# Optimization experiments

Measured on AMD Instinct MI355X. Metric: run time of the kernel, lower is better.

## Reference

```python
import jax, jax.numpy as jnp
import numpy as np
from jax import lax

HEADS = 8
EPS = 1e-5


def _ln2d(x, g, b):
    # LayerNorm over channel axis of BCHW (torch LayerNorm(dim) after b c h w -> b h w c)
    mu = jnp.mean(x, axis=1, keepdims=True)
    var = jnp.mean(jnp.square(x - mu), axis=1, keepdims=True)
    xn = (x - mu) * lax.rsqrt(var + EPS)
    return xn * g[None, :, None, None] + b[None, :, None, None]


def _conv1x1(x, w, b):
    # w: [out_c, in_c]
    return jnp.einsum('bchw,oc->bohw', x, w) + b[None, :, None, None]


def _dwconv3x3(x, w, b):
    # w: [C, 1, 3, 3], depthwise
    y = lax.conv_general_dilated(x, w, window_strides=(1, 1), padding='SAME',
                                 feature_group_count=x.shape[1],
                                 dimension_numbers=('NCHW', 'OIHW', 'NCHW'))
    return y + b[None, :, None, None]


def _gelu(x):
    return jax.nn.gelu(x, approximate=False)


def _linear_attention(x, qkv_w, qkv_b, out_w, out_b):
    B, C, H, W = x.shape
    hd = C // HEADS
    qkv = _conv1x1(x, qkv_w, qkv_b)              # [B, 3C, H, W]
    q, k, v = jnp.split(qkv, 3, axis=1)
    # b (h c) h0 w0 -> b h c (h0 w0)
    q = q.reshape(B, HEADS, hd, H * W)
    k = k.reshape(B, HEADS, hd, H * W)
    v = v.reshape(B, HEADS, hd, H * W)
    q = jax.nn.softmax(q, axis=2)                # over head_dim
    k = jax.nn.softmax(k, axis=3)                # over pixels
    context = jnp.einsum('bhcn,bhdn->bhcd', k, v)  # [B, H, hd, hd]
    out = jnp.einsum('bhcd,bhcn->bhdn', context, q)  # [B, H, hd, N]
    out = out.reshape(B, C, H, W)
    return _conv1x1(out, out_w, out_b)


def _ffn(x, w1, b1, dw_w, dw_b, w2, b2):
    h = _gelu(_conv1x1(x, w1, b1))
    h = _gelu(_dwconv3x3(h, dw_w, dw_b))
    return _conv1x1(h, w2, b2)


def setup_inputs() -> dict:
    key = jax.random.key(0)
    ks = jax.random.split(key, 6)
    B, C, H, W = 4, 192, 256, 256
    hidden = C * 2
    s = 0.02
    return {
        'x': jax.random.normal(ks[0], (B, C, H, W), jnp.float32),
        'ln1_g': jnp.ones((C,), jnp.float32),
        'ln1_b': jnp.zeros((C,), jnp.float32),
        'qkv_w': jax.random.normal(ks[1], (3 * C, C), jnp.float32) * s,
        'qkv_b': jnp.zeros((3 * C,), jnp.float32),
        'out_w': jax.random.normal(ks[2], (C, C), jnp.float32) * s,
        'out_b': jnp.zeros((C,), jnp.float32),
        'ln2_g': jnp.ones((C,), jnp.float32),
        'ln2_b': jnp.zeros((C,), jnp.float32),
        'w1': jax.random.normal(ks[3], (hidden, C), jnp.float32) * s,
        'b1': jnp.zeros((hidden,), jnp.float32),
        'dw_w': jax.random.normal(ks[4], (hidden, 1, 3, 3), jnp.float32) * s,
        'dw_b': jnp.zeros((hidden,), jnp.float32),
        'w2': jax.random.normal(ks[5], (C, hidden), jnp.float32) * s,
        'b2': jnp.zeros((C,), jnp.float32),
    }


def reference(x, ln1_g, ln1_b, qkv_w, qkv_b, out_w, out_b, ln2_g, ln2_b, w1, b1, dw_w, dw_b, w2, b2):
    x = x + _linear_attention(_ln2d(x, ln1_g, ln1_b), qkv_w, qkv_b, out_w, out_b)
    x = x + _ffn(_ln2d(x, ln2_g, ln2_b), w1, b1, dw_w, dw_b, w2, b2)
    return x
```

## Files before the change

kernel.cpp:

```cpp
#include <hip/hip_runtime.h>
#include <math.h>

typedef __attribute__((ext_vector_type(8))) short s8;
typedef __attribute__((ext_vector_type(8))) unsigned short us8;
typedef __attribute__((ext_vector_type(4))) float f4;
typedef __attribute__((ext_vector_type(4))) unsigned short us4;
typedef __attribute__((ext_vector_type(4))) unsigned int u32x4;

#define DEVI __device__ __forceinline__

static const int NPIX = 65536;

DEVI float b2f(unsigned short u) {
    unsigned int v = ((unsigned int)u) << 16;
    float f; __builtin_memcpy(&f, &v, 4); return f;
}
DEVI unsigned short f2b(float f) {
    unsigned int u; __builtin_memcpy(&u, &f, 4);
    unsigned int r = (u + 0x7FFFu + ((u >> 16) & 1u)) >> 16;
    return (unsigned short)r;
}
DEVI float geluf(float x) { return 0.5f * x * (1.0f + erff(x * 0.70710678118f)); }
DEVI float gelu_t(float x) {
    float z = 1.595769122f * (x + 0.044715f * x * x * x);
    return x * __builtin_amdgcn_rcpf(1.0f + __expf(-z));
}
DEVI float rfl(float v) {
    int i; __builtin_memcpy(&i, &v, 4);
    i = __builtin_amdgcn_readfirstlane(i);
    float o; __builtin_memcpy(&o, &i, 4); return o;
}

DEVI void gload_lds16(const unsigned short* g, unsigned short* l) {
    __builtin_amdgcn_global_load_lds(
        (const __attribute__((address_space(1))) unsigned int*)g,
        (__attribute__((address_space(3))) unsigned int*)l,
        16, 0, 0);
}

__global__ __launch_bounds__(256) void lnt_k(const float* __restrict__ X,
                                             const float* __restrict__ gw,
                                             const float* __restrict__ gb,
                                             unsigned short* __restrict__ Out)
{
    const int i = blockIdx.x * 256 + threadIdx.x;
    const int b = i >> 16, px = i & 65535;
    const float* xp = X + (size_t)b * 192 * NPIX + px;

    unsigned int pk[96];
    float sum = 0.f, ssq = 0.f;
    #pragma unroll
    for (int c = 0; c < 192; c++) {
        float v = xp[(size_t)c * NPIX];
        sum += v; ssq += v * v;
        unsigned int h = f2b(v);
        if (c & 1) pk[c >> 1] |= h << 16;
        else       pk[c >> 1] = h;
    }
    float mu = sum * (1.0f / 192.0f);
    float var = ssq * (1.0f / 192.0f) - mu * mu;
    float rs = rsqrtf(var + 1e-5f);

    #pragma unroll
    for (int c2 = 0; c2 < 96; c2++) {
        int c = c2 * 2;
        float lo = b2f((unsigned short)(pk[c2] & 0xFFFF));
        float hi = b2f((unsigned short)(pk[c2] >> 16));
        lo = (lo - mu) * rs * gw[c] + gb[c];
        hi = (hi - mu) * rs * gw[c + 1] + gb[c + 1];
        pk[c2] = (unsigned int)f2b(lo) | ((unsigned int)f2b(hi) << 16);
    }
    u32x4* dst = (u32x4*)(Out + (size_t)i * 192);
    #pragma unroll
    for (int j = 0; j < 6; j++) {
        u32x4 v = { pk[4 * j], pk[4 * j + 1], pk[4 * j + 2], pk[4 * j + 3] };
        dst[j] = v;
    }
}

template<int MODE, int NCHUNK, int UNITS, int NTILE>
__global__ __launch_bounds__(256) void gemm3_k(
    const unsigned short* __restrict__ X, const unsigned short* __restrict__ Wb,
    const float* __restrict__ bias, const void* __restrict__ resid,
    void* __restrict__ Out, int OCTOT, unsigned short* __restrict__ qT)
{
    constexpr int KTOT = UNITS * 192;
    __shared__ unsigned short tile[2][64 * 192];

    const int tid = threadIdx.x;
    const int wave = tid >> 6, lane = tid & 63;
    const int lr = lane & 15, lg = lane >> 4;
    const int xr = lr & 7;

    auto stage = [&](int s, int buf) {
        const int t = s / UNITS, u = s - t * UNITS;
        const int gp0s = (blockIdx.x * NTILE + t) * 64;
        const unsigned short* Xb = X + (size_t)gp0s * KTOT + u * 192;
        #pragma unroll
        for (int j = 0; j < 6; j++) {
            int ci = (wave * 6 + j) * 64 + lane;
            int row = ci / 24;
            int c = ci - row * 24;
            int csw = (c & ~7) | ((c ^ row) & 7);
            gload_lds16(Xb + (size_t)row * KTOT + csw * 8, &tile[buf][ci * 8]);
        }
    };

    stage(0, 0);

    for (int t = 0; t < NTILE; t++) {
        const int gp0 = (blockIdx.x * NTILE + t) * 64;
        const int b = gp0 >> 16;
        const int pxb = gp0 & 65535;

        if constexpr (UNITS == 1) {
            __syncthreads();
            if (t + 1 < NTILE) stage(t + 1, (t + 1) & 1);
            const unsigned short* tb = tile[t & 1];

            #pragma unroll
            for (int cn = 0; cn < NCHUNK; cn++) {
                const int ocb = cn * 192 + wave * 48;
                const unsigned short* wrow = Wb + (size_t)(ocb + lr) * KTOT + lg * 8;
                const bool swapped = (MODE == 1) || (MODE == 3 && cn == 0);

                s8 wf[3][6];
                #pragma unroll
                for (int ot = 0; ot < 3; ot++)
                    #pragma unroll
                    for (int kk = 0; kk < 6; kk++)
                        wf[ot][kk] = *(const s8*)(wrow + (size_t)ot * 16 * KTOT + kk * 32);

                f4 acc[4][3];
                #pragma unroll
                for (int i = 0; i < 4; i++)
                    #pragma unroll
                    for (int j = 0; j < 3; j++) acc[i][j] = (f4)0.0f;

                #pragma unroll
                for (int kk = 0; kk < 6; kk++) {
                    const int kc = kk * 4 + lg;
                    const int kcs = (kc & ~7) | ((kc ^ xr) & 7);
                    s8 a[4];
                    #pragma unroll
                    for (int pt = 0; pt < 4; pt++)
                        a[pt] = *(const s8*)&tb[((pt * 16 + lr) * 24 + kcs) * 8];
                    #pragma unroll
                    for (int ot = 0; ot < 3; ot++)
                        #pragma unroll
                        for (int pt = 0; pt < 4; pt++)
                            acc[pt][ot] = swapped
                                ? __builtin_amdgcn_mfma_f32_16x16x32_bf16(wf[ot][kk], a[pt], acc[pt][ot], 0, 0, 0)
                                : __builtin_amdgcn_mfma_f32_16x16x32_bf16(a[pt], wf[ot][kk], acc[pt][ot], 0, 0, 0);
                }

                if (MODE == 3 && cn == 0) {
                    #pragma unroll
                    for (int pt = 0; pt < 4; pt++) {
                        const int gp = gp0 + pt * 16 + lr;
                        unsigned short* orow = qT + (size_t)gp * 192 + wave * 48 + lg * 4;
                        #pragma unroll
                        for (int ot = 0; ot < 3; ot++) {
                            f4 bi4 = *(const f4*)&bias[wave * 48 + ot * 16 + lg * 4];
                            us4 o;
                            #pragma unroll
                            for (int r = 0; r < 4; r++) o[r] = f2b(acc[pt][ot][r] + bi4[r]);
                            *(us4*)(orow + ot * 16) = o;
                        }
                    }
                } else if (MODE == 3) {
                    #pragma unroll
                    for (int ot = 0; ot < 3; ot++) {
                        const int oc = ocb + ot * 16 + lr;
                        const float bi = bias[oc];
                        const size_t rowoff = ((size_t)b * 384 + (oc - 192)) * NPIX + pxb + lg * 4;
                        #pragma unroll
                        for (int pt = 0; pt < 4; pt++) {
                            us4 o;
                            #pragma unroll
                            for (int r = 0; r < 4; r++) o[r] = f2b(acc[pt][ot][r] + bi);
                            *(us4*)((unsigned short*)Out + rowoff + pt * 16) = o;
                        }
                    }
                } else {
                    #pragma unroll
                    for (int pt = 0; pt < 4; pt++) {
                        const int gp = gp0 + pt * 16 + lr;
                        unsigned short* orow = (unsigned short*)Out + (size_t)gp * OCTOT + ocb + lg * 4;
                        #pragma unroll
                        for (int ot = 0; ot < 3; ot++) {
                            f4 bi4 = *(const f4*)&bias[ocb + ot * 16 + lg * 4];
                            us4 o;
                            #pragma unroll
                            for (int r = 0; r < 4; r++) o[r] = f2b(geluf(acc[pt][ot][r] + bi4[r]));
                            *(us4*)(orow + ot * 16) = o;
                        }
                    }
                }
            }
        } else {
            const int ocb = wave * 48;
            const unsigned short* wrow = Wb + (size_t)(ocb + lr) * KTOT + lg * 8;

            f4 acc[4][3];
            #pragma unroll
            for (int i = 0; i < 4; i++)
                #pragma unroll
                for (int j = 0; j < 3; j++) acc[i][j] = (f4)0.0f;

            #pragma unroll
            for (int u = 0; u < 2; u++) {
                const int s = t * 2 + u;
                __syncthreads();
                if (s + 1 < NTILE * 2) stage(s + 1, (s + 1) & 1);
                const unsigned short* tb = tile[s & 1];

                s8 wf[3][6];
                #pragma unroll
                for (int ot = 0; ot < 3; ot++)
                    #pragma unroll
                    for (int kk = 0; kk < 6; kk++)
                        wf[ot][kk] = *(const s8*)(wrow + (size_t)ot * 16 * KTOT + u * 192 + kk * 32);

                #pragma unroll
                for (int kk = 0; kk < 6; kk++) {
                    const int kc = kk * 4 + lg;
                    const int kcs = (kc & ~7) | ((kc ^ xr) & 7);
                    s8 a[4];
                    #pragma unroll
                    for (int pt = 0; pt < 4; pt++)
                        a[pt] = *(const s8*)&tb[((pt * 16 + lr) * 24 + kcs) * 8];
                    #pragma unroll
                    for (int ot = 0; ot < 3; ot++)
                        #pragma unroll
                        for (int pt = 0; pt < 4; pt++)
                            acc[pt][ot] = __builtin_amdgcn_mfma_f32_16x16x32_bf16(a[pt], wf[ot][kk], acc[pt][ot], 0, 0, 0);
                }
            }

            #pragma unroll
            for (int ot = 0; ot < 3; ot++) {
                const int oc = ocb + ot * 16 + lr;
                const float bi = bias[oc];
                const size_t rowoff = ((size_t)b * 192 + oc) * NPIX + pxb + lg * 4;
                #pragma unroll
                for (int pt = 0; pt < 4; pt++) {
                    if (MODE == 2) {
                        f4 rv = *(const f4*)((const float*)resid + rowoff + pt * 16);
                        f4 o;
                        #pragma unroll
                        for (int r = 0; r < 4; r++) o[r] = acc[pt][ot][r] + bi + rv[r];
                        *(f4*)((float*)Out + rowoff + pt * 16) = o;
                    } else {
                        us4 rv = *(const us4*)((const unsigned short*)resid + rowoff + pt * 16);
                        f4 o;
                        #pragma unroll
                        for (int r = 0; r < 4; r++) o[r] = acc[pt][ot][r] + bi + b2f(rv[r]);
                        *(f4*)((float*)Out + rowoff + pt * 16) = o;
                    }
                }
            }
        }
    }
}

__global__ __launch_bounds__(256) void krow_k(const unsigned short* __restrict__ kv,
                                              float* __restrict__ koff)
{
    int r = blockIdx.x;
    int b = r / 192, ch = r % 192;
    const unsigned short* Kp = kv + ((size_t)b * 384 + ch) * NPIX;
    int tid = threadIdx.x;
    float m0 = -1e30f, s0 = 0.f, m1 = -1e30f, s1 = 0.f;
    for (int i = 0; i < 128; i++) {
        float v0 = b2f(Kp[tid + (size_t)(2 * i) * 256]);
        float v1 = b2f(Kp[tid + (size_t)(2 * i + 1) * 256]);
        if (v0 > m0) { s0 = s0 * __expf(m0 - v0) + 1.f; m0 = v0; }
        else s0 += __expf(v0 - m0);
        if (v1 > m1) { s1 = s1 * __expf(m1 - v1) + 1.f; m1 = v1; }
        else s1 += __expf(v1 - m1);
    }
    float m = fmaxf(m0, m1);
    float s = s0 * __expf(m0 - m) + s1 * __expf(m1 - m);
    __shared__ float ms[256], ss[256];
    ms[tid] = m; ss[tid] = s;
    __syncthreads();
    for (int off = 128; off > 0; off >>= 1) {
        if (tid < off) {
            float m2 = ms[tid + off], s2 = ss[tid + off];
            float M2 = fmaxf(ms[tid], m2);
            ss[tid] = ss[tid] * __expf(ms[tid] - M2) + s2 * __expf(m2 - M2);
            ms[tid] = M2;
        }
        __syncthreads();
    }
    if (tid == 0) koff[r] = ms[0] + logf(ss[0]);
}

__global__ void zero_k(float* __restrict__ p, int n)
{
    int i = blockIdx.x * 256 + threadIdx.x;
    if (i < n) p[i] = 0.f;
}

__global__ void cvt_k(const float* __restrict__ src, unsigned short* __restrict__ dst, int n)
{
    int i = blockIdx.x * 256 + threadIdx.x;
    if (i < n) dst[i] = f2b(src[i]);
}

__global__ __launch_bounds__(256) void context_k(const unsigned short* __restrict__ kv,
                                                 const float* __restrict__ koff,
                                                 float* __restrict__ ctxT)
{
    __shared__ float red[4][64][16];
    int bid = blockIdx.x;
    int bh = bid >> 4, cgrp = bid & 15;
    int b = bh >> 3, h = bh & 7;
    int tid = threadIdx.x;
    int wave = tid >> 6, lane = tid & 63, lr = lane & 15, lg = lane >> 4;
    int chunk = cgrp * 4 + wave;
    size_t nbase = (size_t)chunk * 1024 + lg * 8;

    int c0 = h * 24 + lr;
    int c1 = h * 24 + 16 + lr;
    float ko0 = koff[b * 192 + c0];
    int i1 = b * 192 + c1; if (i1 > 767) i1 = 767;
    float ko1 = koff[i1];
    bool val1 = lr < 8;

    const unsigned short* k0p = kv + ((size_t)b * 384 + c0) * NPIX + nbase;
    const unsigned short* k1p = kv + ((size_t)b * 384 + (c1 > 191 ? 191 : c1)) * NPIX + nbase;
    const unsigned short* v0p = kv + ((size_t)b * 384 + 192 + h * 24 + lr) * NPIX + nbase;
    const unsigned short* v1p = kv + ((size_t)b * 384 + 192 + ((h * 24 + 16 + lr > 191) ? 191 : h * 24 + 16 + lr)) * NPIX + nbase;

    f4 acc[2][2];
    #pragma unroll
    for (int i = 0; i < 2; i++) for (int j = 0; j < 2; j++) acc[i][j] = (f4)0.0f;

    for (int s = 0; s < 32; s++) {
        int off = s * 32;
        s8 kr0 = *(const s8*)(k0p + off);
        s8 kr1 = *(const s8*)(k1p + off);
        s8 vr0 = *(const s8*)(v0p + off);
        s8 vr1 = *(const s8*)(v1p + off);
        s8 p0, p1;
        #pragma unroll
        for (int j = 0; j < 8; j++) {
            p0[j] = (short)f2b(__expf(b2f((unsigned short)kr0[j]) - ko0));
            p1[j] = val1 ? (short)f2b(__expf(b2f((unsigned short)kr1[j]) - ko1)) : (short)0;
        }
        acc[0][0] = __builtin_amdgcn_mfma_f32_16x16x32_bf16(p0, vr0, acc[0][0], 0, 0, 0);
        acc[0][1] = __builtin_amdgcn_mfma_f32_16x16x32_bf16(p0, vr1, acc[0][1], 0, 0, 0);
        acc[1][0] = __builtin_amdgcn_mfma_f32_16x16x32_bf16(p1, vr0, acc[1][0], 0, 0, 0);
        acc[1][1] = __builtin_amdgcn_mfma_f32_16x16x32_bf16(p1, vr1, acc[1][1], 0, 0, 0);
    }
    #pragma unroll
    for (int mt = 0; mt < 2; mt++)
        #pragma unroll
        for (int ct = 0; ct < 2; ct++)
            #pragma unroll
            for (int r = 0; r < 4; r++)
                red[wave][lane][mt * 8 + ct * 4 + r] = acc[mt][ct][r];
    __syncthreads();

    if (wave == 0) {
        float* base = ctxT + (size_t)(b * 8 + h) * 1024;
        #pragma unroll
        for (int j = 0; j < 16; j++) {
            float sum = red[0][lane][j] + red[1][lane][j] + red[2][lane][j] + red[3][lane][j];
            int mt = j >> 3, ct = (j >> 2) & 1, r = j & 3;
            int c = mt * 16 + lg * 4 + r;
            int d = ct * 16 + lr;
            atomicAdd(base + d * 32 + c, sum);
        }
    }
}

template<bool BIGWS>
__global__ __launch_bounds__(256) void qctx_proj_k(
    const unsigned short* __restrict__ qT, const float* __restrict__ ctxT,
    const unsigned short* __restrict__ outWb, const float* __restrict__ outBias,
    const float* __restrict__ xres, float* __restrict__ Out,
    unsigned short* __restrict__ x2b,
    const float* __restrict__ ln2g, const float* __restrict__ ln2b,
    unsigned short* __restrict__ xnt)
{
    __shared__ unsigned short outp[64][200];
    __shared__ float lnS[4][64], lnQ[4][64];

    int tid = threadIdx.x, bid = blockIdx.x;
    int b = bid >> 10, n0 = (bid & 1023) * 64;
    int wave = tid >> 6, lane = tid & 63, lr = lane & 15, lg = lane >> 4;
    const size_t bpx = (size_t)b << 16;

    #pragma unroll
    for (int hh = 0; hh < 2; hh++) {
        int h = wave * 2 + hh;
        s8 cf[2];
        #pragma unroll
        for (int mt = 0; mt < 2; mt++) {
            const float* cp = ctxT + ((size_t)(b * 8 + h) * 32 + mt * 16 + lr) * 32 + lg * 8;
            s8 a;
            #pragma unroll
            for (int j = 0; j < 8; j++) a[j] = (short)f2b(cp[j]);
            cf[mt] = a;
        }
        #pragma unroll
        for (int nt = 0; nt < 4; nt++) {
            int n = nt * 16 + lr;
            s8 bfq = (s8)0;
            float sown = 0.f;
            if (lg < 3) {
                us8 qv = *(const us8*)(qT + (bpx + n0 + n) * 192 + h * 24 + lg * 8);
                #pragma unroll
                for (int j = 0; j < 8; j++) {
                    float e = __expf(b2f((unsigned short)qv[j]));
                    sown += e;
                    bfq[j] = (short)f2b(e);
                }
            }
            float den = sown;
            den += __shfl_xor(den, 16);
            den += __shfl_xor(den, 32);
            f4 z = (f4)0.0f;
            f4 d0 = __builtin_amdgcn_mfma_f32_16x16x32_bf16(cf[0], bfq, z, 0, 0, 0);
            f4 d1 = __builtin_amdgcn_mfma_f32_16x16x32_bf16(cf[1], bfq, z, 0, 0, 0);
            float sinv = 1.0f / den;
            us4 w0;
            #pragma unroll
            for (int r = 0; r < 4; r++) w0[r] = f2b(d0[r] * sinv);
            *(us4*)&outp[n][h * 24 + lg * 4] = w0;
            if (lg < 2) {
                us4 w1;
                #pragma unroll
                for (int r = 0; r < 4; r++) w1[r] = f2b(d1[r] * sinv);
                *(us4*)&outp[n][h * 24 + 16 + lg * 4] = w1;
            }
        }
    }
    __syncthreads();

    f4 acc[4][3];
    #pragma unroll
    for (int i = 0; i < 4; i++) for (int j = 0; j < 3; j++) acc[i][j] = (f4)0.0f;
    #pragma unroll
    for (int k0 = 0; k0 < 192; k0 += 32) {
        s8 bf[4];
        #pragma unroll
        for (int pt = 0; pt < 4; pt++)
            bf[pt] = *(const s8*)&outp[pt * 16 + lr][k0 + lg * 8];
        #pragma unroll
        for (int ot = 0; ot < 3; ot++) {
            s8 af = *(const s8*)&outWb[(size_t)(wave * 48 + ot * 16 + lr) * 192 + k0 + lg * 8];
            #pragma unroll
            for (int pt = 0; pt < 4; pt++)
                acc[pt][ot] = __builtin_amdgcn_mfma_f32_16x16x32_bf16(bf[pt], af, acc[pt][ot], 0, 0, 0);
        }
    }

    float sP[4][4], qP[4][4];
    #pragma unroll
    for (int pt = 0; pt < 4; pt++)
        #pragma unroll
        for (int r = 0; r < 4; r++) { sP[pt][r] = 0.f; qP[pt][r] = 0.f; }

    #pragma unroll
    for (int ot = 0; ot < 3; ot++) {
        const int oc = wave * 48 + ot * 16 + lr;
        const float bi = outBias[oc];
        const size_t rowbase = ((size_t)b * 192 + oc) * NPIX + n0 + lg * 4;
        #pragma unroll
        for (int pt = 0; pt < 4; pt++) {
            f4 rv = *(const f4*)(xres + rowbase + pt * 16);
            f4 v;
            #pragma unroll
            for (int r = 0; r < 4; r++) {
                v[r] = acc[pt][ot][r] + bi + rv[r];
                sP[pt][r] += v[r]; qP[pt][r] += v[r] * v[r];
            }
            acc[pt][ot] = v;
            if (BIGWS) {
                us4 o;
                #pragma unroll
                for (int r = 0; r < 4; r++) o[r] = f2b(v[r]);
                *(us4*)(x2b + rowbase + pt * 16) = o;
            } else {
                *(f4*)(Out + rowbase + pt * 16) = v;
            }
        }
    }
    #pragma unroll
    for (int pt = 0; pt < 4; pt++)
        #pragma unroll
        for (int r = 0; r < 4; r++) {
            float s = sP[pt][r], q = qP[pt][r];
            s += __shfl_xor(s, 1); s += __shfl_xor(s, 2);
            s += __shfl_xor(s, 4); s += __shfl_xor(s, 8);
            q += __shfl_xor(q, 1); q += __shfl_xor(q, 2);
            q += __shfl_xor(q, 4); q += __shfl_xor(q, 8);
            sP[pt][r] = s; qP[pt][r] = q;
        }
    if (lr == 0) {
        #pragma unroll
        for (int pt = 0; pt < 4; pt++)
            #pragma unroll
            for (int r = 0; r < 4; r++) {
                lnS[wave][pt * 16 + lg * 4 + r] = sP[pt][r];
                lnQ[wave][pt * 16 + lg * 4 + r] = qP[pt][r];
            }
    }
    __syncthreads();

    float lgv[3], lbv[3];
    #pragma unroll
    for (int ot = 0; ot < 3; ot++) {
        int oc = wave * 48 + ot * 16 + lr;
        lgv[ot] = ln2g[oc]; lbv[ot] = ln2b[oc];
    }
    #pragma unroll
    for (int pt = 0; pt < 4; pt++) {
        float mu4[4], rs4[4];
        #pragma unroll
        for (int r = 0; r < 4; r++) {
            int px = pt * 16 + lg * 4 + r;
            float S = lnS[0][px] + lnS[1][px] + lnS[2][px] + lnS[3][px];
            float Qq = lnQ[0][px] + lnQ[1][px] + lnQ[2][px] + lnQ[3][px];
            float mu = S * (1.0f / 192.0f);
            float var = Qq * (1.0f / 192.0f) - mu * mu;
            mu4[r] = mu; rs4[r] = rsqrtf(var + 1e-5f);
        }
        #pragma unroll
        for (int ot = 0; ot < 3; ot++) {
            int oc = wave * 48 + ot * 16 + lr;
            #pragma unroll
            for (int r = 0; r < 4; r++) {
                int px = pt * 16 + lg * 4 + r;
                float xn = (acc[pt][ot][r] - mu4[r]) * rs4[r] * lgv[ot] + lbv[ot];
                outp[px][oc] = f2b(xn);
            }
        }
    }
    __syncthreads();

    #pragma unroll
    for (int q = 0; q < 6; q++) {
        int idx = q * 256 + tid;
        int px = idx / 24, c8 = idx % 24;
        us8 v = *(const us8*)&outp[px][c8 * 8];
        *(us8*)(xnt + (bpx + n0 + px) * 192 + c8 * 8) = v;
    }
}

__global__ __launch_bounds__(256) void dwconv_t2_k(
    const unsigned short* __restrict__ h1t, const float* __restrict__ w,
    const float* __restrict__ bias, unsigned short* __restrict__ h2t)
{
    __shared__ unsigned short ring[4 * 4 * 66 * 8];
    const int bz = blockIdx.z;
    const int b = bz / 12, cb = (bz % 12) * 32;
    const int y0 = blockIdx.y * 8, x0 = blockIdx.x * 64;
    const int tid = threadIdx.x;
    const int x = tid & 63, cg = tid >> 6;
    const int c0 = cb + cg * 8;
    const size_t bbase = (size_t)b << 16;

    float wr[9][8], bi[8];
    #pragma unroll
    for (int i = 0; i < 8; i++) {
        #pragma unroll
        for (int j = 0; j < 9; j++) wr[j][i] = rfl(w[(c0 + i) * 9 + j]);
        bi[i] = rfl(bias[c0 + i]);
    }

    const us8 zz = {0, 0, 0, 0, 0, 0, 0, 0};

    auto stage_row = [&](int gy, int s) {
        unsigned short* ldsrow = &ring[((s * 4 + cg) * 66) * 8];
        if (gy >= 0 && gy <= 255) {
            us8 ev = zz;
            if (x == 0 && x0 > 0)
                ev = *(const us8*)(h1t + (bbase + gy * 256 + x0 - 1) * 384 + c0);
            if (x == 63 && x0 + 64 < 256)
                ev = *(const us8*)(h1t + (bbase + gy * 256 + x0 + 64) * 384 + c0);
            gload_lds16(h1t + (bbase + gy * 256 + x0 + x) * 384 + c0,
                        ldsrow + (1 + x) * 8);
            if (x == 0)  *(us8*)&ldsrow[0]      = ev;
            if (x == 63) *(us8*)&ldsrow[65 * 8] = ev;
        } else {
            *(us8*)&ldsrow[(1 + x) * 8] = zz;
            if (x == 0)  *(us8*)&ldsrow[0]      = zz;
            if (x == 63) *(us8*)&ldsrow[65 * 8] = zz;
        }
    };

    stage_row(y0 - 1, 0);
    stage_row(y0,     1);
    stage_row(y0 + 1, 2);
    __syncthreads();

    #pragma unroll
    for (int y = 0; y < 8; y++) {
        if (y < 7) stage_row(y0 + y + 2, (y + 3) & 3);

        float a[8];
        #pragma unroll
        for (int i = 0; i < 8; i++) a[i] = bi[i];
        #pragma unroll
        for (int t = 0; t < 3; t++) {
            const int s = (y + t) & 3;
            const unsigned short* rp = &ring[((s * 4 + cg) * 66 + x) * 8];
            us8 L = *(const us8*)(rp);
            us8 C = *(const us8*)(rp + 8);
            us8 R = *(const us8*)(rp + 16);
            #pragma unroll
            for (int i = 0; i < 8; i++) {
                a[i] += wr[t * 3 + 0][i] * b2f(L[i]);
                a[i] += wr[t * 3 + 1][i] * b2f(C[i]);
                a[i] += wr[t * 3 + 2][i] * b2f(R[i]);
            }
        }
        us8 ov;
        #pragma unroll
        for (int i = 0; i < 8; i++) ov[i] = f2b(gelu_t(a[i]));
        *(us8*)(h2t + (bbase + (y0 + y) * 256 + x0 + x) * 384 + c0) = ov;

        __syncthreads();
    }
}

extern "C" void kernel_launch(void* const* d_in, const int* in_sizes, int n_in,
                              void* d_out, int out_size, void* d_ws, size_t ws_size,
                              hipStream_t stream)
{
    const float* x    = (const float*)d_in[0];
    const float* ln1g = (const float*)d_in[1];
    const float* ln1b = (const float*)d_in[2];
    const float* qkvw = (const float*)d_in[3];
    const float* qkvb = (const float*)d_in[4];
    const float* outw = (const float*)d_in[5];
    const float* outb = (const float*)d_in[6];
    const float* ln2g = (const float*)d_in[7];
    const float* ln2b = (const float*)d_in[8];
    const float* w1   = (const float*)d_in[9];
    const float* b1   = (const float*)d_in[10];
    const float* dww  = (const float*)d_in[11];
    const float* dwb  = (const float*)d_in[12];
    const float* w2   = (const float*)d_in[13];
    const float* b2   = (const float*)d_in[14];
    float* out = (float*)d_out;

    char* ws = (char*)d_ws;
    unsigned short* kv  = (unsigned short*)ws;
    unsigned short* h1t = (unsigned short*)ws;
    unsigned short* h2t = (unsigned short*)(ws + (size_t)201326592);
    unsigned short* qT  = (unsigned short*)(ws + (size_t)201326592);
    unsigned short* xnt = (unsigned short*)(ws + (size_t)301989888);
    size_t off = (size_t)402653184;
    float* koff = (float*)(ws + off); off += 4096;
    float* ctxT = (float*)(ws + off); off += 131072;
    unsigned short* qkvwb = (unsigned short*)(ws + off); off += 221184;
    unsigned short* outwb = (unsigned short*)(ws + off); off += 73728 * 2;
    unsigned short* w1b   = (unsigned short*)(ws + off); off += 147456;
    unsigned short* w2b   = (unsigned short*)(ws + off); off += 147456;
    off = (off + 255) & ~(size_t)255;
    unsigned short* x2b = (unsigned short*)(ws + off);
    const bool bigws = ws_size >= off + (size_t)100663296;

    cvt_k<<<(110592 + 255) / 256, 256, 0, stream>>>(qkvw, qkvwb, 110592);
    cvt_k<<<(36864 + 255) / 256, 256, 0, stream>>>(outw, outwb, 36864);
    cvt_k<<<(73728 + 255) / 256, 256, 0, stream>>>(w1, w1b, 73728);
    cvt_k<<<(73728 + 255) / 256, 256, 0, stream>>>(w2, w2b, 73728);

    lnt_k<<<1024, 256, 0, stream>>>(x, ln1g, ln1b, xnt);

    gemm3_k<3, 3, 1, 4><<<1024, 256, 0, stream>>>(xnt, qkvwb, qkvb, nullptr, kv, 384, qT);

    krow_k<<<768, 256, 0, stream>>>(kv, koff);

    zero_k<<<128, 256, 0, stream>>>(ctxT, 32768);
    context_k<<<512, 256, 0, stream>>>(kv, koff, ctxT);

    if (bigws)
        qctx_proj_k<true><<<4096, 256, 0, stream>>>(qT, ctxT, outwb, outb, x, out,
                                                    x2b, ln2g, ln2b, xnt);
    else
        qctx_proj_k<false><<<4096, 256, 0, stream>>>(qT, ctxT, outwb, outb, x, out,
                                                     x2b, ln2g, ln2b, xnt);

    gemm3_k<1, 2, 1, 4><<<1024, 256, 0, stream>>>(xnt, w1b, b1, nullptr, h1t, 384, nullptr);

    dwconv_t2_k<<<dim3(4, 32, 48), 256, 0, stream>>>(h1t, dww, dwb, h2t);

    if (bigws)
        gemm3_k<4, 1, 2, 4><<<1024, 256, 0, stream>>>(h2t, w2b, b2, x2b, out, 192, nullptr);
    else
        gemm3_k<2, 1, 2, 4><<<1024, 256, 0, stream>>>(h2t, w2b, b2, out, out, 192, nullptr);
}
```

Before: 971.7 us.

## Process two pixel tiles per block in qctx_proj with async Q staging; taller dwconv tiles

The fused q-softmax/context/out-projection/LN2 kernel now handles two 64-pixel tiles per block. Each tile's Q slice is prefetched into a swizzled LDS buffer with direct global-to-LDS loads, and the next tile's Q is staged while the current tile's projection runs. The out-projection weight fragments are held in registers per tile instead of being reloaded inside the k loop. Separately, the depthwise conv block now covers 16 rows instead of 8, which reduces halo row reloads. The cost is higher register and LDS pressure and fewer blocks in flight.

```diff
diff --git a/kernel.cpp b/kernel.cpp
--- a/kernel.cpp
+++ b/kernel.cpp
@@ -386,169 +386,201 @@
     const float* __restrict__ ln2g, const float* __restrict__ ln2b,
     unsigned short* __restrict__ xnt)
 {
+    __shared__ unsigned short qtile[64 * 192];
     __shared__ unsigned short outp[64][200];
     __shared__ float lnS[4][64], lnQ[4][64];
 
     int tid = threadIdx.x, bid = blockIdx.x;
-    int b = bid >> 10, n0 = (bid & 1023) * 64;
+    int b = bid >> 9;
+    int base_n0 = (bid & 511) * 128;
     int wave = tid >> 6, lane = tid & 63, lr = lane & 15, lg = lane >> 4;
     const size_t bpx = (size_t)b << 16;
 
-    #pragma unroll
-    for (int hh = 0; hh < 2; hh++) {
-        int h = wave * 2 + hh;
-        s8 cf[2];
-        #pragma unroll
-        for (int mt = 0; mt < 2; mt++) {
-            const float* cp = ctxT + ((size_t)(b * 8 + h) * 32 + mt * 16 + lr) * 32 + lg * 8;
-            s8 a;
-            #pragma unroll
-            for (int j = 0; j < 8; j++) a[j] = (short)f2b(cp[j]);
-            cf[mt] = a;
-        }
-        #pragma unroll
-        for (int nt = 0; nt < 4; nt++) {
-            int n = nt * 16 + lr;
-            s8 bfq = (s8)0;
-            float sown = 0.f;
-            if (lg < 3) {
-                us8 qv = *(const us8*)(qT + (bpx + n0 + n) * 192 + h * 24 + lg * 8);
-                #pragma unroll
-                for (int j = 0; j < 8; j++) {
-                    float e = __expf(b2f((unsigned short)qv[j]));
-                    sown += e;
-                    bfq[j] = (short)f2b(e);
-                }
-            }
-            float den = sown;
-            den += __shfl_xor(den, 16);
-            den += __shfl_xor(den, 32);
-            f4 z = (f4)0.0f;
-            f4 d0 = __builtin_amdgcn_mfma_f32_16x16x32_bf16(cf[0], bfq, z, 0, 0, 0);
-            f4 d1 = __builtin_amdgcn_mfma_f32_16x16x32_bf16(cf[1], bfq, z, 0, 0, 0);
-            float sinv = 1.0f / den;
-            us4 w0;
-            #pragma unroll
-            for (int r = 0; r < 4; r++) w0[r] = f2b(d0[r] * sinv);
-            *(us4*)&outp[n][h * 24 + lg * 4] = w0;
-            if (lg < 2) {
-                us4 w1;
-                #pragma unroll
-                for (int r = 0; r < 4; r++) w1[r] = f2b(d1[r] * sinv);
-                *(us4*)&outp[n][h * 24 + 16 + lg * 4] = w1;
-            }
-        }
-    }
-    __syncthreads();
-
-    f4 acc[4][3];
-    #pragma unroll
-    for (int i = 0; i < 4; i++) for (int j = 0; j < 3; j++) acc[i][j] = (f4)0.0f;
-    #pragma unroll
-    for (int k0 = 0; k0 < 192; k0 += 32) {
-        s8 bf[4];
+    auto stage_q = [&](int t) {
+        const unsigned short* Qb = qT + (bpx + base_n0 + t * 64) * 192;
+        #pragma unroll
+        for (int j = 0; j < 6; j++) {
+            int ci = (wave * 6 + j) * 64 + lane;
+            int row = ci / 24;
+            int c = ci - row * 24;
+            int csw = (c & ~7) | ((c ^ row) & 7);
+            gload_lds16(Qb + (size_t)row * 192 + csw * 8, &qtile[ci * 8]);
+        }
+    };
+
+    stage_q(0);
+
+    for (int t = 0; t < 2; t++) {
+        const int n0 = base_n0 + t * 64;
+
+        __syncthreads();
+
+        s8 wf[3][6];
+        #pragma unroll
+        for (int ot = 0; ot < 3; ot++)
+            #pragma unroll
+            for (int kk = 0; kk < 6; kk++)
+                wf[ot][kk] = *(const s8*)&outWb[(size_t)(wave * 48 + ot * 16 + lr) * 192 + kk * 32 + lg * 8];
+
+        #pragma unroll
+        for (int hh = 0; hh < 2; hh++) {
+            int h = wave * 2 + hh;
+            s8 cf[2];
+            #pragma unroll
+            for (int mt = 0; mt < 2; mt++) {
+                const float* cp = ctxT + ((size_t)(b * 8 + h) * 32 + mt * 16 + lr) * 32 + lg * 8;
+                s8 a;
+                #pragma unroll
+                for (int j = 0; j < 8; j++) a[j] = (short)f2b(cp[j]);
+                cf[mt] = a;
+            }
+            #pragma unroll
+            for (int nt = 0; nt < 4; nt++) {
+                int n = nt * 16 + lr;
+                s8 bfq = (s8)0;
+                float sown = 0.f;
+                if (lg < 3) {
+                    int kc = h * 3 + lg;
+                    int kcs = (kc & ~7) | ((kc ^ (n & 7)) & 7);
+                    us8 qv = *(const us8*)&qtile[(n * 24 + kcs) * 8];
+                    #pragma unroll
+                    for (int j = 0; j < 8; j++) {
+                        float e = __expf(b2f((unsigned short)qv[j]));
+                        sown += e;
+                        bfq[j] = (short)f2b(e);
+                    }
+                }
+                float den = sown;
+                den += __shfl_xor(den, 16);
+                den += __shfl_xor(den, 32);
+                f4 z = (f4)0.0f;
+                f4 d0 = __builtin_amdgcn_mfma_f32_16x16x32_bf16(cf[0], bfq, z, 0, 0, 0);
+                f4 d1 = __builtin_amdgcn_mfma_f32_16x16x32_bf16(cf[1], bfq, z, 0, 0, 0);
+                float sinv = 1.0f / den;
+                us4 w0;
+                #pragma unroll
+                for (int r = 0; r < 4; r++) w0[r] = f2b(d0[r] * sinv);
+                *(us4*)&outp[n][h * 24 + lg * 4] = w0;
+                if (lg < 2) {
+                    us4 w1;
+                    #pragma unroll
+                    for (int r = 0; r < 4; r++) w1[r] = f2b(d1[r] * sinv);
+                    *(us4*)&outp[n][h * 24 + 16 + lg * 4] = w1;
+                }
+            }
+        }
+        __syncthreads();
+
+        if (t == 0) stage_q(1);
+
+        f4 acc[4][3];
+        #pragma unroll
+        for (int i = 0; i < 4; i++) for (int j = 0; j < 3; j++) acc[i][j] = (f4)0.0f;
+        #pragma unroll
+        for (int kk = 0; kk < 6; kk++) {
+            const int k0 = kk * 32;
+            s8 bf[4];
+            #pragma unroll
+            for (int pt = 0; pt < 4; pt++)
+                bf[pt] = *(const s8*)&outp[pt * 16 + lr][k0 + lg * 8];
+            #pragma unroll
+            for (int ot = 0; ot < 3; ot++)
+                #pragma unroll
+                for (int pt = 0; pt < 4; pt++)
+                    acc[pt][ot] = __builtin_amdgcn_mfma_f32_16x16x32_bf16(bf[pt], wf[ot][kk], acc[pt][ot], 0, 0, 0);
+        }
+
+        float sP[4][4], qP[4][4];
         #pragma unroll
         for (int pt = 0; pt < 4; pt++)
-            bf[pt] = *(const s8*)&outp[pt * 16 + lr][k0 + lg * 8];
+            #pragma unroll
+            for (int r = 0; r < 4; r++) { sP[pt][r] = 0.f; qP[pt][r] = 0.f; }
+
         #pragma unroll
         for (int ot = 0; ot < 3; ot++) {
-            s8 af = *(const s8*)&outWb[(size_t)(wave * 48 + ot * 16 + lr) * 192 + k0 + lg * 8];
+            const int oc = wave * 48 + ot * 16 + lr;
+            const float bi = outBias[oc];
+            const size_t rowbase = ((size_t)b * 192 + oc) * NPIX + n0 + lg * 4;
+            #pragma unroll
+            for (int pt = 0; pt < 4; pt++) {
+                f4 rv = *(const f4*)(xres + rowbase + pt * 16);
+                f4 v;
+                #pragma unroll
+                for (int r = 0; r < 4; r++) {
+                    v[r] = acc[pt][ot][r] + bi + rv[r];
+                    sP[pt][r] += v[r]; qP[pt][r] += v[r] * v[r];
+                }
+                acc[pt][ot] = v;
+                if (BIGWS) {
+                    us4 o;
+                    #pragma unroll
+                    for (int r = 0; r < 4; r++) o[r] = f2b(v[r]);
+                    *(us4*)(x2b + rowbase + pt * 16) = o;
+                } else {
+                    *(f4*)(Out + rowbase + pt * 16) = v;
+                }
+            }
+        }
+        #pragma unroll
+        for (int pt = 0; pt < 4; pt++)
+            #pragma unroll
+            for (int r = 0; r < 4; r++) {
+                float s = sP[pt][r], q = qP[pt][r];
+                s += __shfl_xor(s, 1); s += __shfl_xor(s, 2);
+                s += __shfl_xor(s, 4); s += __shfl_xor(s, 8);
+                q += __shfl_xor(q, 1); q += __shfl_xor(q, 2);
+                q += __shfl_xor(q, 4); q += __shfl_xor(q, 8);
+                sP[pt][r] = s; qP[pt][r] = q;
+            }
+        if (lr == 0) {
             #pragma unroll
             for (int pt = 0; pt < 4; pt++)
-                acc[pt][ot] = __builtin_amdgcn_mfma_f32_16x16x32_bf16(bf[pt], af, acc[pt][ot], 0, 0, 0);
-        }
-    }
-
-    float sP[4][4], qP[4][4];
-    #pragma unroll
-    for (int pt = 0; pt < 4; pt++)
-        #pragma unroll
-        for (int r = 0; r < 4; r++) { sP[pt][r] = 0.f; qP[pt][r] = 0.f; }
-
-    #pragma unroll
-    for (int ot = 0; ot < 3; ot++) {
-        const int oc = wave * 48 + ot * 16 + lr;
-        const float bi = outBias[oc];
-        const size_t rowbase = ((size_t)b * 192 + oc) * NPIX + n0 + lg * 4;
-        #pragma unroll
-        for (int pt = 0; pt < 4; pt++) {
-            f4 rv = *(const f4*)(xres + rowbase + pt * 16);
-            f4 v;
-            #pragma unroll
-            for (int r = 0; r < 4; r++) {
-                v[r] = acc[pt][ot][r] + bi + rv[r];
-                sP[pt][r] += v[r]; qP[pt][r] += v[r] * v[r];
-            }
-            acc[pt][ot] = v;
-            if (BIGWS) {
-                us4 o;
-                #pragma unroll
-                for (int r = 0; r < 4; r++) o[r] = f2b(v[r]);
-                *(us4*)(x2b + rowbase + pt * 16) = o;
-            } else {
-                *(f4*)(Out + rowbase + pt * 16) = v;
-            }
-        }
-    }
-    #pragma unroll
-    for (int pt = 0; pt < 4; pt++)
-        #pragma unroll
-        for (int r = 0; r < 4; r++) {
-            float s = sP[pt][r], q = qP[pt][r];
-            s += __shfl_xor(s, 1); s += __shfl_xor(s, 2);
-            s += __shfl_xor(s, 4); s += __shfl_xor(s, 8);
-            q += __shfl_xor(q, 1); q += __shfl_xor(q, 2);
-            q += __shfl_xor(q, 4); q += __shfl_xor(q, 8);
-            sP[pt][r] = s; qP[pt][r] = q;
-        }
-    if (lr == 0) {
-        #pragma unroll
-        for (int pt = 0; pt < 4; pt++)
-            #pragma unroll
-            for (int r = 0; r < 4; r++) {
-                lnS[wave][pt * 16 + lg * 4 + r] = sP[pt][r];
-                lnQ[wave][pt * 16 + lg * 4 + r] = qP[pt][r];
-            }
-    }
-    __syncthreads();
-
-    float lgv[3], lbv[3];
-    #pragma unroll
-    for (int ot = 0; ot < 3; ot++) {
-        int oc = wave * 48 + ot * 16 + lr;
-        lgv[ot] = ln2g[oc]; lbv[ot] = ln2b[oc];
-    }
-    #pragma unroll
-    for (int pt = 0; pt < 4; pt++) {
-        float mu4[4], rs4[4];
-        #pragma unroll
-        for (int r = 0; r < 4; r++) {
-            int px = pt * 16 + lg * 4 + r;
-            float S = lnS[0][px] + lnS[1][px] + lnS[2][px] + lnS[3][px];
-            float Qq = lnQ[0][px] + lnQ[1][px] + lnQ[2][px] + lnQ[3][px];
-            float mu = S * (1.0f / 192.0f);
-            float var = Qq * (1.0f / 192.0f) - mu * mu;
-            mu4[r] = mu; rs4[r] = rsqrtf(var + 1e-5f);
-        }
+                #pragma unroll
+                for (int r = 0; r < 4; r++) {
+                    lnS[wave][pt * 16 + lg * 4 + r] = sP[pt][r];
+                    lnQ[wave][pt * 16 + lg * 4 + r] = qP[pt][r];
+                }
+        }
+        __syncthreads();
+
+        float lgv[3], lbv[3];
         #pragma unroll
         for (int ot = 0; ot < 3; ot++) {
             int oc = wave * 48 + ot * 16 + lr;
+            lgv[ot] = ln2g[oc]; lbv[ot] = ln2b[oc];
+        }
+        #pragma unroll
+        for (int pt = 0; pt < 4; pt++) {
+            float mu4[4], rs4[4];
             #pragma unroll
             for (int r = 0; r < 4; r++) {
                 int px = pt * 16 + lg * 4 + r;
-                float xn = (acc[pt][ot][r] - mu4[r]) * rs4[r] * lgv[ot] + lbv[ot];
-                outp[px][oc] = f2b(xn);
-            }
-        }
-    }
-    __syncthreads();
-
-    #pragma unroll
-    for (int q = 0; q < 6; q++) {
-        int idx = q * 256 + tid;
-        int px = idx / 24, c8 = idx % 24;
-        us8 v = *(const us8*)&outp[px][c8 * 8];
-        *(us8*)(xnt + (bpx + n0 + px) * 192 + c8 * 8) = v;
+                float S = lnS[0][px] + lnS[1][px] + lnS[2][px] + lnS[3][px];
+                float Qq = lnQ[0][px] + lnQ[1][px] + lnQ[2][px] + lnQ[3][px];
+                float mu = S * (1.0f / 192.0f);
+                float var = Qq * (1.0f / 192.0f) - mu * mu;
+                mu4[r] = mu; rs4[r] = rsqrtf(var + 1e-5f);
+            }
+            #pragma unroll
+            for (int ot = 0; ot < 3; ot++) {
+                int oc = wave * 48 + ot * 16 + lr;
+                #pragma unroll
+                for (int r = 0; r < 4; r++) {
+                    int px = pt * 16 + lg * 4 + r;
+                    float xn = (acc[pt][ot][r] - mu4[r]) * rs4[r] * lgv[ot] + lbv[ot];
+                    outp[px][oc] = f2b(xn);
+                }
+            }
+        }
+        __syncthreads();
+
+        #pragma unroll
+        for (int q = 0; q < 6; q++) {
+            int idx = q * 256 + tid;
+            int px = idx / 24, c8 = idx % 24;
+            us8 v = *(const us8*)&outp[px][c8 * 8];
+            *(us8*)(xnt + (bpx + n0 + px) * 192 + c8 * 8) = v;
+        }
     }
 }
 
@@ -559,7 +591,7 @@
     __shared__ unsigned short ring[4 * 4 * 66 * 8];
     const int bz = blockIdx.z;
     const int b = bz / 12, cb = (bz % 12) * 32;
-    const int y0 = blockIdx.y * 8, x0 = blockIdx.x * 64;
+    const int y0 = blockIdx.y * 16, x0 = blockIdx.x * 64;
     const int tid = threadIdx.x;
     const int x = tid & 63, cg = tid >> 6;
     const int c0 = cb + cg * 8;
@@ -600,8 +632,8 @@
     __syncthreads();
 
     #pragma unroll
-    for (int y = 0; y < 8; y++) {
-        if (y < 7) stage_row(y0 + y + 2, (y + 3) & 3);
+    for (int y = 0; y < 16; y++) {
+        if (y < 15) stage_row(y0 + y + 2, (y + 3) & 3);
 
         float a[8];
         #pragma unroll
@@ -682,15 +714,15 @@
     context_k<<<512, 256, 0, stream>>>(kv, koff, ctxT);
 
     if (bigws)
-        qctx_proj_k<true><<<4096, 256, 0, stream>>>(qT, ctxT, outwb, outb, x, out,
+        qctx_proj_k<true><<<2048, 256, 0, stream>>>(qT, ctxT, outwb, outb, x, out,
                                                     x2b, ln2g, ln2b, xnt);
     else
-        qctx_proj_k<false><<<4096, 256, 0, stream>>>(qT, ctxT, outwb, outb, x, out,
+        qctx_proj_k<false><<<2048, 256, 0, stream>>>(qT, ctxT, outwb, outb, x, out,
                                                      x2b, ln2g, ln2b, xnt);
 
     gemm3_k<1, 2, 1, 4><<<1024, 256, 0, stream>>>(xnt, w1b, b1, nullptr, h1t, 384, nullptr);
 
-    dwconv_t2_k<<<dim3(4, 32, 48), 256, 0, stream>>>(h1t, dww, dwb, h2t);
+    dwconv_t2_k<<<dim3(4, 16, 48), 256, 0, stream>>>(h1t, dww, dwb, h2t);
 
     if (bigws)
         gemm3_k<4, 1, 2, 4><<<1024, 256, 0, stream>>>(h2t, w2b, b2, x2b, out, 192, nullptr);
```

Result: slower. 1.002 ms (+3.1%).
